# Performance work log

Hardware: AMD Instinct MI355X
Metric: run time of the kernel (lower is better)

## Reference

```python
import jax, jax.numpy as jnp
import numpy as np

B, M, N, R, FIN, D, H = 16, 512, 512, 8, 4, 256, 4
DH = D // H
LGAT = 2
TF_RATE, THRESH = 0.9, 2.0
GAT_W, ORG_W, DET_W = 0.5, 0.5, 0.5


def setup_inputs() -> dict:
    key = jax.random.key(0)
    ks = jax.random.split(key, 16)
    g = lambda k, shp, fan: jax.random.normal(k, shp, jnp.float32) / np.sqrt(fan)
    inp = {
        'tracks': jax.random.normal(ks[0], (B, M, R, FIN), jnp.float32),
        'detections': jax.random.normal(ks[1], (B, N, FIN), jnp.float32),
        'tracklet_marks': jax.random.randint(ks[2], (B,), M // 2, M + 1, jnp.int32),
        'detection_marks': jax.random.randint(ks[3], (B,), N // 2, N + 1, jnp.int32),
        'feat_W1': g(ks[4], (FIN, D), FIN),
        'feat_b1': jnp.zeros((D,), jnp.float32),
        'feat_W2': g(ks[5], (D, D), D),
        'feat_b2': jnp.zeros((D,), jnp.float32),
        'enc_Wqkv': g(ks[6], (D, 3 * D), D),
        'enc_Wo': g(ks[7], (D, D), D),
        'enc_ff1': g(ks[8], (D, 4 * D), D),
        'enc_ff2': g(ks[9], (4 * D, D), 4 * D),
        'gat_W': g(ks[10], (LGAT, D, D), D),
        'gat_a': g(ks[11], (LGAT, 2, H, DH), DH),
        'det_gat_W': g(ks[12], (LGAT, D, D), D),
        'det_gat_a': g(ks[13], (LGAT, 2, H, DH), DH),
        'cls_Wq': g(ks[14], (2, D, D), D),
        'cls_Wk': g(ks[15], (2, D, D), D),
    }
    return inp


def _ln(x):
    m = jnp.mean(x, -1, keepdims=True)
    v = jnp.var(x, -1, keepdims=True)
    return (x - m) * jax.lax.rsqrt(v + 1e-5)


def _feat(x, W1, b1, W2, b2):
    return jax.nn.elu(x @ W1 + b1) @ W2 + b2


def _encoder(x, Wqkv, Wo, ff1, ff2):
    # x: [T, R, D] -> one pre-LN transformer layer over the rewind axis
    T = x.shape[0]
    h = _ln(x)
    qkv = (h @ Wqkv).reshape(T, R, 3, H, DH)
    q, k, v = qkv[:, :, 0], qkv[:, :, 1], qkv[:, :, 2]
    att = jax.nn.softmax(jnp.einsum('trhd,tshd->thrs', q, k) / np.sqrt(DH), axis=-1)
    o = jnp.einsum('thrs,tshd->trhd', att, v).reshape(T, R, D) @ Wo
    x = x + o
    return x + jax.nn.relu(_ln(x) @ ff1) @ ff2


def _gat(x, adj, W, a):
    # x: [B, Nn, D]; adj: [B, Nn, Nn] bool; a: [2, H, DH]
    b, nn_, _ = x.shape
    h = (x @ W).reshape(b, nn_, H, DH)
    src = jnp.einsum('bnhd,hd->bnh', h, a[0])
    dst = jnp.einsum('bnhd,hd->bnh', h, a[1])
    e = jax.nn.leaky_relu(src[:, :, None, :] + dst[:, None, :, :], 0.2)  # [B,Nn,Nn,H]
    e = jnp.where(adj[..., None], e, -1e9)
    alpha = jax.nn.softmax(e, axis=2)
    out = jnp.einsum('bijh,bjhd->bihd', alpha, h).reshape(b, nn_, D)
    return jax.nn.elu(out)


def _scores(x, adj_f, Wq, Wk):
    s = jax.nn.sigmoid(jnp.einsum('bid,bjd->bij', x @ Wq, x @ Wk) / np.sqrt(D))
    return s * adj_f


def _forward(tracks, detections, tracklet_marks, detection_marks,
             feat_W1, feat_b1, feat_W2, feat_b2,
             enc_Wqkv, enc_Wo, enc_ff1, enc_ff2,
             gat_W, gat_a, det_gat_W, det_gat_a, cls_Wq, cls_Wk):
    tr_emb = _feat(tracks, feat_W1, feat_b1, feat_W2, feat_b2)      # [B,M,R,D]
    det_emb = _feat(detections, feat_W1, feat_b1, feat_W2, feat_b2)  # [B,N,D]

    enc = _encoder(tr_emb.reshape(B * M, R, D), enc_Wqkv, enc_Wo, enc_ff1, enc_ff2)
    enc = enc.reshape(B, M, R, D)
    predicted = tr_emb[:, :, 0, :] + TF_RATE * enc[:, :, 0, :]       # [B,M,D]

    tmask = jnp.arange(M)[None, :] < tracklet_marks[:, None]
    dmask = jnp.arange(N)[None, :] < detection_marks[:, None]

    pos = jnp.concatenate([tracks[:, :, 0, :2], detections[:, :, :2]], axis=1)  # [B,M+N,2]
    vmask = jnp.concatenate([tmask, dmask], axis=1)
    dist = jnp.linalg.norm(pos[:, :, None, :] - pos[:, None, :, :], axis=-1)
    adj = (dist < THRESH) & vmask[:, :, None] & vmask[:, None, :]
    adj_f = adj.astype(jnp.float32)

    feat0 = jnp.concatenate([predicted, det_emb], axis=1)  # [B,M+N,D]
    x = feat0
    for l in range(LGAT):
        x = GAT_W * _gat(x, adj, gat_W[l], gat_a[l]) + ORG_W * feat0
    scores = _scores(x, adj_f, cls_Wq[0], cls_Wk[0])       # [B,M+N,M+N]
    asso_results = scores[:, :M, M:]                        # track->det block

    pd = detections[:, :, :2]
    dist_d = jnp.linalg.norm(pd[:, :, None, :] - pd[:, None, :, :], axis=-1)
    adj_d = (dist_d < THRESH) & dmask[:, :, None] & dmask[:, None, :]
    adj_d_f = adj_d.astype(jnp.float32)

    xd = det_emb
    for l in range(LGAT):
        xd = DET_W * _gat(xd, adj_d, det_gat_W[l], det_gat_a[l]) + ORG_W * det_emb
    det_scores = _scores(xd, adj_d_f, cls_Wq[1], cls_Wk[1])
    det_scores = det_scores * (1.0 - jnp.eye(N, dtype=jnp.float32))  # zero_diag

    return scores, det_scores, asso_results


def reference(tracks, detections, tracklet_marks, detection_marks,
              feat_W1, feat_b1, feat_W2, feat_b2,
              enc_Wqkv, enc_Wo, enc_ff1, enc_ff2,
              gat_W, gat_a, det_gat_W, det_gat_a, cls_Wq, cls_Wk):
    return _forward(tracks, detections, tracklet_marks, detection_marks,
                    feat_W1, feat_b1, feat_W2, feat_b2,
                    enc_Wqkv, enc_Wo, enc_ff1, enc_ff2,
                    gat_W, gat_a, det_gat_W, det_gat_a, cls_Wq, cls_Wk)
```

## Files before the change

kernel.cpp:

```cpp
#include <hip/hip_runtime.h>
#include <math.h>


typedef __bf16 bf16;
typedef __bf16 bf16x8 __attribute__((ext_vector_type(8)));
typedef __bf16 bf16x4 __attribute__((ext_vector_type(4)));
typedef float f32x4 __attribute__((ext_vector_type(4)));

__device__ __forceinline__ float bf2f(bf16 x) { return (float)x; }
__device__ __forceinline__ bf16 f2bf(float x) { return (bf16)x; }

__device__ __forceinline__ unsigned encf(float f) {
    unsigned u = __float_as_uint(f);
    return (u & 0x80000000u) ? ~u : (u | 0x80000000u);
}
__device__ __forceinline__ float decf(unsigned u) {
    return (u & 0x80000000u) ? __uint_as_float(u & 0x7fffffffu)
                             : __uint_as_float(~u);
}

__device__ __forceinline__ bool node_adj(float4 a, float4 c) {
    float dx = a.x - c.x, dy = a.y - c.y;
    return (sqrtf(dx * dx + dy * dy) + a.z + c.z) < 2.0f;
}

struct PrepEnt { const float* src; long dofs; int R; int C; int tstart; };
struct PrepTab { PrepEnt e[13]; };

__global__ __launch_bounds__(256) void k_prep(PrepTab tab, bf16* __restrict__ dst)
{
    __shared__ float tile[32][33];
    const int tid = blockIdx.x;
    int k = 0;
    #pragma unroll
    for (int q = 1; q < 13; ++q) if (tid >= tab.e[q].tstart) k = q;
    PrepEnt E = tab.e[k];
    const int local = tid - E.tstart;
    const int cT = E.C >> 5;
    const int tr = local / cT, tc = local - tr * cT;
    const int r0 = tr << 5, c0 = tc << 5;
    const int t = threadIdx.x;
    {
        int r = t >> 3, cq = (t & 7) * 4;
        *(float4*)&tile[r][cq] = *(const float4*)(E.src + (long)(r0 + r) * E.C + c0 + cq);
    }
    __syncthreads();
    {
        int c = t >> 3, rq = (t & 7) * 4;
        bf16x4 o;
        o[0] = f2bf(tile[rq + 0][c]); o[1] = f2bf(tile[rq + 1][c]);
        o[2] = f2bf(tile[rq + 2][c]); o[3] = f2bf(tile[rq + 3][c]);
        *(bf16x4*)(dst + E.dofs + (long)(c0 + c) * E.R + r0 + rq) = o;
    }
}

__device__ __forceinline__ void gemm_bt_mn(const bf16* __restrict__ A, int lda,
                                           const bf16* __restrict__ BT, int ldb,
                                           int K, int m0, int n0, f32x4 acc[4])
{
    __shared__ bf16 As[64][40];
    __shared__ bf16 Bs[64][40];
    const int t = threadIdx.x;
    const int lane = t & 63, wv = t >> 6, lr = lane & 15, kq = lane >> 4;
    const int arow = t >> 2, acol = (t & 3) * 8;
    for (int k0 = 0; k0 < K; k0 += 32) {
        __syncthreads();
        *(uint4*)&As[arow][acol] = *(const uint4*)(A + (long)(m0 + arow) * lda + k0 + acol);
        *(uint4*)&Bs[arow][acol] = *(const uint4*)(BT + (long)(n0 + arow) * ldb + k0 + acol);
        __syncthreads();
        bf16x8 af = *(const bf16x8*)&As[wv * 16 + lr][kq * 8];
        #pragma unroll
        for (int nt = 0; nt < 4; ++nt) {
            bf16x8 bfr = *(const bf16x8*)&Bs[nt * 16 + lr][kq * 8];
            acc[nt] = __builtin_amdgcn_mfma_f32_16x16x32_bf16(af, bfr, acc[nt], 0, 0, 0);
        }
    }
}

__device__ __forceinline__ void gemm_bt(const bf16* __restrict__ A, int lda,
                                        const bf16* __restrict__ BT, int ldb,
                                        int K, f32x4 acc[4])
{
    gemm_bt_mn(A, lda, BT, ldb, K, blockIdx.y * 64, blockIdx.x * 64, acc);
}

__device__ __forceinline__ void gemm128_core(const bf16* __restrict__ A, int lda,
                                             const bf16* __restrict__ BT, int ldb,
                                             int m0, int n0, int K, f32x4 acc[2][8])
{
    __shared__ bf16 As[128][40];
    __shared__ bf16 Bs[128][40];
    const int t = threadIdx.x;
    const int lane = t & 63, wv = t >> 6, lr = lane & 15, kq = lane >> 4;
    const int srow = t >> 1, scol = (t & 1) * 16;
    for (int k0 = 0; k0 < K; k0 += 32) {
        __syncthreads();
        {
            const bf16* ap = A + (long)(m0 + srow) * lda + k0 + scol;
            *(uint4*)&As[srow][scol] = *(const uint4*)ap;
            *(uint4*)&As[srow][scol + 8] = *(const uint4*)(ap + 8);
            const bf16* bp = BT + (long)(n0 + srow) * ldb + k0 + scol;
            *(uint4*)&Bs[srow][scol] = *(const uint4*)bp;
            *(uint4*)&Bs[srow][scol + 8] = *(const uint4*)(bp + 8);
        }
        __syncthreads();
        bf16x8 af[2];
        af[0] = *(const bf16x8*)&As[wv * 32 + lr][kq * 8];
        af[1] = *(const bf16x8*)&As[wv * 32 + 16 + lr][kq * 8];
        #pragma unroll
        for (int nt = 0; nt < 8; ++nt) {
            bf16x8 bfr = *(const bf16x8*)&Bs[nt * 16 + lr][kq * 8];
            acc[0][nt] = __builtin_amdgcn_mfma_f32_16x16x32_bf16(af[0], bfr, acc[0][nt], 0, 0, 0);
            acc[1][nt] = __builtin_amdgcn_mfma_f32_16x16x32_bf16(af[1], bfr, acc[1][nt], 0, 0, 0);
        }
    }
}

__global__ __launch_bounds__(256) void k_gemm128_bf16(
    const bf16* __restrict__ A, int lda,
    const bf16* __restrict__ BT, int ldb,
    bf16* __restrict__ out, int ldo, int K, int relu)
{
    f32x4 acc[2][8] = {};
    const int m0 = blockIdx.y * 128, n0 = blockIdx.x * 128;
    gemm128_core(A, lda, BT, ldb, m0, n0, K, acc);
    const int lane = threadIdx.x & 63, wv = threadIdx.x >> 6;
    const int lr = lane & 15, kq = lane >> 4;
    #pragma unroll
    for (int mt = 0; mt < 2; ++mt) {
        #pragma unroll
        for (int nt = 0; nt < 8; ++nt) {
            int col = n0 + nt * 16 + lr;
            #pragma unroll
            for (int i = 0; i < 4; ++i) {
                int row = m0 + wv * 32 + mt * 16 + kq * 4 + i;
                float v = acc[mt][nt][i];
                if (relu) v = fmaxf(v, 0.f);
                out[(long)row * ldo + col] = f2bf(v);
            }
        }
    }
}

__global__ __launch_bounds__(256) void k_kvq(
    const bf16* __restrict__ hln, const bf16* __restrict__ WqkvT,
    bf16* __restrict__ kv, bf16* __restrict__ q)
{
    const int bid = blockIdx.x;
    const bf16* A; const bf16* BT; bf16* out;
    int lda, ldo, m0, n0;
    if (bid < 2048) {
        A = hln; lda = 256; BT = WqkvT + 65536;
        m0 = (bid >> 2) * 128; n0 = (bid & 3) * 128;
        out = kv; ldo = 512;
    } else {
        int t2 = bid - 2048;
        A = hln; lda = 2048; BT = WqkvT;
        m0 = (t2 >> 1) * 128; n0 = (t2 & 1) * 128;
        out = q; ldo = 256;
    }
    f32x4 acc[2][8] = {};
    gemm128_core(A, lda, BT, 256, m0, n0, 256, acc);
    const int lane = threadIdx.x & 63, wv = threadIdx.x >> 6;
    const int lr = lane & 15, kq = lane >> 4;
    #pragma unroll
    for (int mt = 0; mt < 2; ++mt) {
        #pragma unroll
        for (int nt = 0; nt < 8; ++nt) {
            int col = n0 + nt * 16 + lr;
            #pragma unroll
            for (int i = 0; i < 4; ++i) {
                int row = m0 + wv * 32 + mt * 16 + kq * 4 + i;
                out[(long)row * ldo + col] = f2bf(acc[mt][nt][i]);
            }
        }
    }
}

__global__ __launch_bounds__(256) void k_logits(
    const bf16* __restrict__ xqkm, const bf16* __restrict__ xqkd,
    const unsigned long long* __restrict__ adjmM,
    const unsigned long long* __restrict__ adjmD,
    float* __restrict__ out, float* __restrict__ asso)
{
    const int bid = blockIdx.x;
    const bf16* xqk; float* ob; const unsigned long long* adjm;
    int ldo, nN, nC, flags, m0, n0, z;
    long sAz, sOz;
    if (bid < 1024) {
        z = bid >> 6; int r = bid & 63;
        m0 = (r >> 3) * 128; n0 = (r & 7) * 128;
        xqk = xqkm; sAz = 524288; ob = out; ldo = 1024; sOz = 1048576;
        adjm = adjmM; nN = 1024; nC = 16; flags = 1;
    } else {
        int b2 = bid - 1024;
        z = b2 >> 4; int r = b2 & 15;
        m0 = (r >> 2) * 128; n0 = (r & 3) * 128;
        xqk = xqkd; sAz = 262144; ob = out + 16777216; ldo = 512; sOz = 262144;
        adjm = adjmD; nN = 512; nC = 8; flags = 2;
    }
    f32x4 acc[2][8] = {};
    gemm128_core(xqk + z * sAz, 512, xqk + z * sAz + 256, 512, m0, n0, 256, acc);
    const int lane = threadIdx.x & 63, wv = threadIdx.x >> 6;
    const int lr = lane & 15, kq = lane >> 4;
    float* obz = ob + z * sOz;
    #pragma unroll
    for (int mt = 0; mt < 2; ++mt) {
        #pragma unroll
        for (int i = 0; i < 4; ++i) {
            int row = m0 + wv * 32 + mt * 16 + kq * 4 + i;
            unsigned long long w0 = adjm[((long)z * nN + row) * nC + (n0 >> 6)];
            unsigned long long w1 = adjm[((long)z * nN + row) * nC + (n0 >> 6) + 1];
            #pragma unroll
            for (int nt = 0; nt < 8; ++nt) {
                int col = n0 + nt * 16 + lr;
                int bp = nt * 16 + lr;
                bool adj = (bp < 64) ? ((w0 >> bp) & 1ull) : ((w1 >> (bp - 64)) & 1ull);
                if ((flags & 2) && row == col) adj = false;
                float v = 0.f;
                if (adj) v = 1.f / (1.f + __expf(-acc[mt][nt][i] * 0.0625f));
                obz[(long)row * ldo + col] = v;
                if ((flags & 1) && row < 512 && col >= 512)
                    asso[(long)z * 262144 + (long)row * 512 + (col - 512)] = v;
            }
        }
    }
}

__global__ __launch_bounds__(256) void k_cls(
    const bf16* __restrict__ Am, const bf16* __restrict__ QKm, bf16* __restrict__ outm,
    const bf16* __restrict__ Ad, const bf16* __restrict__ QKd, bf16* __restrict__ outd)
{
    int by = blockIdx.y;
    const bf16 *A, *BT; bf16* out;
    if (by < 256) { A = Am; BT = QKm; out = outm; }
    else          { by -= 256; A = Ad; BT = QKd; out = outd; }
    f32x4 acc[4] = {};
    const int m0 = by * 64, n0 = blockIdx.x * 64;
    gemm_bt_mn(A, 256, BT, 256, 256, m0, n0, acc);
    const int lane = threadIdx.x & 63, wv = threadIdx.x >> 6;
    const int lr = lane & 15, kq = lane >> 4;
    #pragma unroll
    for (int nt = 0; nt < 4; ++nt) {
        int col = n0 + nt * 16 + lr;
        #pragma unroll
        for (int i = 0; i < 4; ++i) {
            int row = m0 + wv * 16 + kq * 4 + i;
            out[(long)row * 512 + col] = f2bf(acc[nt][i]);
        }
    }
}

__global__ __launch_bounds__(256) void k_gemm_pred(
    const bf16* __restrict__ A, int lda,
    const bf16* __restrict__ BT, int ldb,
    const float* __restrict__ res1, const float* __restrict__ res2,
    float* __restrict__ outf, bf16* __restrict__ outb, int K)
{
    f32x4 acc[4] = {};
    gemm_bt(A, lda, BT, ldb, K, acc);
    const int lane = threadIdx.x & 63, wv = threadIdx.x >> 6;
    const int lr = lane & 15, kq = lane >> 4;
    const int m0 = blockIdx.y * 64, n0 = blockIdx.x * 64;
    #pragma unroll
    for (int nt = 0; nt < 4; ++nt) {
        int col = n0 + nt * 16 + lr;
        #pragma unroll
        for (int i = 0; i < 4; ++i) {
            int row = m0 + wv * 16 + kq * 4 + i;
            float v = res1[(long)row * 256 + col]
                    + 0.9f * (res2[(long)row * 256 + col] + acc[nt][i]);
            long drow = (long)row + ((row >> 9) << 9);
            long o = drow * 256 + col;
            outf[o] = v;
            outb[o] = f2bf(v);
        }
    }
}

__global__ __launch_bounds__(256) void k_featgemm(
    const float* __restrict__ tracks, const float* __restrict__ dets,
    const float* __restrict__ W1, const float* __restrict__ b1,
    const bf16* __restrict__ W2T, const float* __restrict__ b2,
    bf16* __restrict__ hln, float* __restrict__ emb_r0_f,
    float* __restrict__ feat0_f, bf16* __restrict__ feat0_b,
    bf16* __restrict__ demb_b)
{
    __shared__ float xr[64][4];
    __shared__ float w1s[4][256];
    __shared__ float b1s[256];
    __shared__ bf16 As[64][40];
    __shared__ bf16 Bs[256][40];
    const int t = threadIdx.x;
    const int m0 = blockIdx.x * 64;
    if (t < 64) {
        int gr = m0 + t;
        const float* sp = (gr < 65536) ? (tracks + (long)gr * 4)
                                       : (dets + (long)(gr - 65536) * 4);
        *(float4*)&xr[t][0] = *(const float4*)sp;
    }
    w1s[0][t] = W1[t];       w1s[1][t] = W1[256 + t];
    w1s[2][t] = W1[512 + t]; w1s[3][t] = W1[768 + t];
    b1s[t] = b1[t];
    const int arow = t >> 2, acol = (t & 3) * 8;
    const int lane = t & 63, wv = t >> 6, lr = lane & 15, kq = lane >> 4;
    f32x4 acc[16] = {};
    __syncthreads();
    for (int k0 = 0; k0 < 256; k0 += 32) {
        __syncthreads();
        #pragma unroll
        for (int j = 0; j < 8; ++j) {
            int c = k0 + acol + j;
            float v = fmaf(xr[arow][0], w1s[0][c],
                      fmaf(xr[arow][1], w1s[1][c],
                      fmaf(xr[arow][2], w1s[2][c],
                      fmaf(xr[arow][3], w1s[3][c], b1s[c]))));
            v = v > 0.f ? v : (__expf(v) - 1.f);
            As[arow][acol + j] = f2bf(v);
        }
        #pragma unroll
        for (int rr = 0; rr < 4; ++rr) {
            int n = rr * 64 + (t >> 2);
            *(uint4*)&Bs[n][acol] = *(const uint4*)(W2T + (long)n * 256 + k0 + acol);
        }
        __syncthreads();
        bf16x8 af = *(const bf16x8*)&As[wv * 16 + lr][kq * 8];
        #pragma unroll
        for (int nt = 0; nt < 16; ++nt) {
            bf16x8 bfr = *(const bf16x8*)&Bs[nt * 16 + lr][kq * 8];
            acc[nt] = __builtin_amdgcn_mfma_f32_16x16x32_bf16(af, bfr, acc[nt], 0, 0, 0);
        }
    }
    if (m0 < 65536) {
        #pragma unroll
        for (int nt = 0; nt < 16; ++nt) {
            int col = nt * 16 + lr;
            float bv = b2[col];
            #pragma unroll
            for (int i = 0; i < 4; ++i) {
                int gr = m0 + wv * 16 + kq * 4 + i;
                float v = acc[nt][i] + bv;
                if ((gr & 7) == 0) emb_r0_f[(long)(gr >> 3) * 256 + col] = v;
                acc[nt][i] = bf2f(f2bf(v));
            }
        }
        float mean[4], rstd[4];
        #pragma unroll
        for (int i = 0; i < 4; ++i) {
            float s1 = 0.f, s2 = 0.f;
            #pragma unroll
            for (int nt = 0; nt < 16; ++nt) {
                float v = acc[nt][i];
                s1 += v; s2 += v * v;
            }
            #pragma unroll
            for (int o = 1; o < 16; o <<= 1) {
                s1 += __shfl_xor(s1, o, 64);
                s2 += __shfl_xor(s2, o, 64);
            }
            float mu = s1 * (1.f / 256.f);
            mean[i] = mu;
            rstd[i] = rsqrtf(fmaxf(s2 * (1.f / 256.f) - mu * mu, 0.f) + 1e-5f);
        }
        #pragma unroll
        for (int nt = 0; nt < 16; ++nt) {
            int col = nt * 16 + lr;
            #pragma unroll
            for (int i = 0; i < 4; ++i) {
                int gr = m0 + wv * 16 + kq * 4 + i;
                hln[(long)gr * 256 + col] = f2bf((acc[nt][i] - mean[i]) * rstd[i]);
            }
        }
    } else {
        #pragma unroll
        for (int nt = 0; nt < 16; ++nt) {
            int col = nt * 16 + lr;
            float bv = b2[col];
            #pragma unroll
            for (int i = 0; i < 4; ++i) {
                int gr = m0 + wv * 16 + kq * 4 + i;
                float v = acc[nt][i] + bv;
                int dr = gr - 65536;
                long drow = ((long)(dr >> 9) << 10) + 512 + (dr & 511);
                feat0_f[drow * 256 + col] = v;
                feat0_b[drow * 256 + col] = f2bf(v);
                demb_b[(long)dr * 256 + col] = f2bf(v);
            }
        }
    }
}

__global__ __launch_bounds__(256) void k_adjmask(
    const float4* __restrict__ nodes,
    unsigned long long* __restrict__ adjm_main,
    unsigned long long* __restrict__ adjm_det)
{
    int bi, nN, nLog, nodeOfs;
    unsigned long long* adjm;
    if (blockIdx.x < 16384) { bi = blockIdx.x; nN = 1024; nLog = 10; nodeOfs = 0; adjm = adjm_main; }
    else { bi = blockIdx.x - 16384; nN = 512; nLog = 9; nodeOfs = 512; adjm = adjm_det; }
    const int b = bi >> nLog;
    const int i = bi & (nN - 1);
    const float4* nb = nodes + b * 1024 + nodeOfs;
    const float4 ni = nb[i];
    const int t = threadIdx.x;
    const int w = t >> 6, lane = t & 63;
    const int nC = nN >> 6;
    for (int it = 0; it * 256 < nN; ++it) {
        int j = it * 256 + t;
        bool adj = node_adj(ni, nb[j]);
        unsigned long long mask = __ballot(adj);
        if (lane == 0) adjm[(long)bi * nC + it * 4 + w] = mask;
    }
}

__global__ __launch_bounds__(256) void k_addres_ln(
    const bf16* __restrict__ A, const bf16* __restrict__ BT,
    const float* __restrict__ res1,
    float* __restrict__ x2out, bf16* __restrict__ h2)
{
    __shared__ bf16 As[64][40];
    __shared__ bf16 Bs[256][40];
    const int t = threadIdx.x;
    const int m0 = blockIdx.x * 64;
    const int arow = t >> 2, acol = (t & 3) * 8;
    const int lane = t & 63, wv = t >> 6, lr = lane & 15, kq = lane >> 4;
    f32x4 acc[16] = {};
    for (int k0 = 0; k0 < 256; k0 += 32) {
        __syncthreads();
        *(uint4*)&As[arow][acol] = *(const uint4*)(A + (long)(m0 + arow) * 256 + k0 + acol);
        #pragma unroll
        for (int rr = 0; rr < 4; ++rr) {
            int n = rr * 64 + (t >> 2);
            *(uint4*)&Bs[n][acol] = *(const uint4*)(BT + (long)n * 256 + k0 + acol);
        }
        __syncthreads();
        bf16x8 af = *(const bf16x8*)&As[wv * 16 + lr][kq * 8];
        #pragma unroll
        for (int nt = 0; nt < 16; ++nt) {
            bf16x8 bfr = *(const bf16x8*)&Bs[nt * 16 + lr][kq * 8];
            acc[nt] = __builtin_amdgcn_mfma_f32_16x16x32_bf16(af, bfr, acc[nt], 0, 0, 0);
        }
    }
    float mean[4], rstd[4];
    #pragma unroll
    for (int i = 0; i < 4; ++i) {
        int row = m0 + wv * 16 + kq * 4 + i;
        float s1 = 0.f, s2 = 0.f;
        #pragma unroll
        for (int nt = 0; nt < 16; ++nt) {
            float v = res1[(long)row * 256 + nt * 16 + lr] + acc[nt][i];
            acc[nt][i] = v;
            s1 += v; s2 += v * v;
        }
        #pragma unroll
        for (int o = 1; o < 16; o <<= 1) {
            s1 += __shfl_xor(s1, o, 64);
            s2 += __shfl_xor(s2, o, 64);
        }
        float mu = s1 * (1.f / 256.f);
        mean[i] = mu;
        rstd[i] = rsqrtf(fmaxf(s2 * (1.f / 256.f) - mu * mu, 0.f) + 1e-5f);
    }
    #pragma unroll
    for (int nt = 0; nt < 16; ++nt) {
        int col = nt * 16 + lr;
        #pragma unroll
        for (int i = 0; i < 4; ++i) {
            int row = m0 + wv * 16 + kq * 4 + i;
            float v = acc[nt][i];
            x2out[(long)row * 256 + col] = v;
            h2[(long)row * 256 + col] = f2bf((v - mean[i]) * rstd[i]);
        }
    }
}

__global__ __launch_bounds__(256) void k_attn(
    const bf16* __restrict__ q, const bf16* __restrict__ kv,
    bf16* __restrict__ o0)
{
    const long t = blockIdx.x;
    const int h = threadIdx.x >> 6;
    const int lane = threadIdx.x & 63;
    const int s = lane >> 3;
    const int dg = lane & 7;
    const bf16* qp = q + t * 256 + h * 64 + dg * 8;
    const bf16* kp = kv + (t * 8 + s) * 512 + h * 64 + dg * 8;
    float p = 0.f;
    #pragma unroll
    for (int e = 0; e < 8; ++e) p += bf2f(qp[e]) * bf2f(kp[e]);
    p += __shfl_xor(p, 1, 64);
    p += __shfl_xor(p, 2, 64);
    p += __shfl_xor(p, 4, 64);
    float sc = p * 0.125f;
    float w[8];
    float mx = -1e30f;
    #pragma unroll
    for (int s2 = 0; s2 < 8; ++s2) { w[s2] = __shfl(sc, s2 * 8, 64); mx = fmaxf(mx, w[s2]); }
    float sum = 0.f;
    #pragma unroll
    for (int s2 = 0; s2 < 8; ++s2) { w[s2] = __expf(w[s2] - mx); sum += w[s2]; }
    float rs = 1.f / sum;
    float acc = 0.f;
    const bf16* vp = kv + (t * 8) * 512 + 256 + h * 64 + lane;
    #pragma unroll
    for (int s2 = 0; s2 < 8; ++s2) acc += w[s2] * bf2f(vp[(long)s2 * 512]);
    o0[t * 256 + h * 64 + lane] = f2bf(acc * rs);
}

__global__ __launch_bounds__(256) void k_nodes(
    const float* __restrict__ tracks, const float* __restrict__ dets,
    const int* __restrict__ tm, const int* __restrict__ dm,
    float4* __restrict__ nodes, unsigned* __restrict__ maxd_all)
{
    int idx = blockIdx.x * 256 + threadIdx.x;
    if (blockIdx.x == 0) maxd_all[threadIdx.x] = 0x007fffffu;
    int b = idx >> 10;
    int i = idx & 1023;
    float x, y;
    int valid;
    if (i < 512) {
        long o = (long)(b * 512 + i) * 32;
        x = tracks[o]; y = tracks[o + 1];
        valid = (i < tm[b]) ? 1 : 0;
    } else {
        int n = i - 512;
        long o = (long)(b * 512 + n) * 4;
        x = dets[o]; y = dets[o + 1];
        valid = (n < dm[b]) ? 1 : 0;
    }
    nodes[idx] = make_float4(x, y, valid ? 0.f : 1e9f, 0.f);
}

__global__ __launch_bounds__(256) void k_gemmT_src(
    const bf16* __restrict__ WTm, const bf16* __restrict__ Xm, bf16* __restrict__ hgTm,
    const float* __restrict__ avm, float* __restrict__ srcm, float* __restrict__ dstm,
    unsigned* __restrict__ mxm,
    const bf16* __restrict__ WTd, const bf16* __restrict__ Xd, bf16* __restrict__ hgTd,
    const float* __restrict__ avd, float* __restrict__ srcd, float* __restrict__ dstd,
    unsigned* __restrict__ mxd)
{
    __shared__ float sred[4][2][64];
    int bx = blockIdx.x;
    const bf16 *WT, *X; bf16* hgT; const float* av;
    float *src, *dst; unsigned* mx; int nN, nLog;
    if (bx < 256) { WT = WTm; X = Xm; hgT = hgTm; av = avm; src = srcm; dst = dstm; mx = mxm; nN = 1024; nLog = 10; }
    else { bx -= 256; WT = WTd; X = Xd; hgT = hgTd; av = avd; src = srcd; dst = dstd; mx = mxd; nN = 512; nLog = 9; }
    const int h = blockIdx.y;
    const int d0 = h * 64, n0 = bx * 64;
    f32x4 acc[4] = {};
    gemm_bt_mn(WT, 256, X, 256, 256, d0, n0, acc);
    const int t = threadIdx.x, lane = t & 63, wv = t >> 6, lr = lane & 15, kq = lane >> 4;
    float a0c[4], a1c[4];
    *(float4*)a0c = *(const float4*)(av + h * 64 + wv * 16 + kq * 4);
    *(float4*)a1c = *(const float4*)(av + 256 + h * 64 + wv * 16 + kq * 4);
    #pragma unroll
    for (int nt = 0; nt < 4; ++nt) {
        int node = n0 + nt * 16 + lr;
        int b = node >> nLog;
        int j = node & (nN - 1);
        float p0 = 0.f, p1 = 0.f;
        #pragma unroll
        for (int i = 0; i < 4; ++i) {
            int d = d0 + wv * 16 + kq * 4 + i;
            bf16 vb = f2bf(acc[nt][i]);
            hgT[((long)(b * 256 + d) << nLog) + j] = vb;
            float vr = bf2f(vb);
            p0 += vr * a0c[i];
            p1 += vr * a1c[i];
        }
        p0 += __shfl_xor(p0, 16, 64); p0 += __shfl_xor(p0, 32, 64);
        p1 += __shfl_xor(p1, 16, 64); p1 += __shfl_xor(p1, 32, 64);
        if (kq == 0) { sred[wv][0][nt * 16 + lr] = p0; sred[wv][1][nt * 16 + lr] = p1; }
    }
    __syncthreads();
    if (t < 64) {
        float s0 = sred[0][0][t] + sred[1][0][t] + sred[2][0][t] + sred[3][0][t];
        float s1 = sred[0][1][t] + sred[1][1][t] + sred[2][1][t] + sred[3][1][t];
        int node = n0 + t;
        src[(long)node * 4 + h] = s0;
        dst[(long)node * 4 + h] = s1;
        float m = s1;
        #pragma unroll
        for (int o = 32; o; o >>= 1) m = fmaxf(m, __shfl_xor(m, o, 64));
        if (t == 0) atomicMax(&mx[(n0 >> nLog) * 4 + h], encf(m));
    }
}

__global__ __launch_bounds__(256) void k_gatagg2(
    const bf16* __restrict__ hgTm, const unsigned long long* __restrict__ adjmM,
    const float4* __restrict__ srcM, const unsigned* __restrict__ mxM,
    const float4* __restrict__ dstM, const float* __restrict__ resM, bf16* __restrict__ outM,
    const bf16* __restrict__ hgTd, const unsigned long long* __restrict__ adjmD,
    const float4* __restrict__ srcD, const unsigned* __restrict__ mxD,
    const float4* __restrict__ dstD, const float* __restrict__ resD, bf16* __restrict__ outD)
{
    __shared__ float dstT[4][1024];
    __shared__ unsigned int adjW[32][33];
    int bid = blockIdx.x;
    const bf16* hgT; const unsigned long long* adjm; const float4* srcv;
    const unsigned* mxp; const float4* dstv; const float* res; bf16* outb; int nN;
    if (bid < 512) { hgT = hgTm; adjm = adjmM; srcv = srcM; mxp = mxM; dstv = dstM; res = resM; outb = outM; nN = 1024; }
    else { bid -= 512; hgT = hgTd; adjm = adjmD; srcv = srcD; mxp = mxD; dstv = dstD; res = resD; outb = outD; nN = 512; }
    const int t = threadIdx.x;
    const int nblk = nN >> 5;
    const int b = bid / nblk;
    const int i0 = (bid - b * nblk) << 5;
    const int nC = nN >> 6;
    for (int j = t; j < nN; j += 256) {
        float4 dj = dstv[(long)b * nN + j];
        dstT[0][j] = dj.x; dstT[1][j] = dj.y; dstT[2][j] = dj.z; dstT[3][j] = dj.w;
    }
    for (int idx = t; idx < 32 * nC; idx += 256) {
        int r = idx / nC, c = idx - r * nC;
        unsigned long long v = adjm[((long)b * nN + i0 + r) * nC + c];
        adjW[r][c * 2] = (unsigned)v;
        adjW[r][c * 2 + 1] = (unsigned)(v >> 32);
    }
    __syncthreads();
    const int h = t >> 6, lane = t & 63, lr = lane & 15, kq = lane >> 4;
    const float mdh = decf(mxp[b * 4 + h]);
    float s_r[2], m_r[2], psum[2] = {0.f, 0.f};
    #pragma unroll
    for (int mt = 0; mt < 2; ++mt) {
        long idx = (long)b * nN + i0 + mt * 16 + lr;
        s_r[mt] = ((const float*)(srcv + idx))[h];
        float tmp = s_r[mt] + mdh;
        m_r[mt] = fmaxf(tmp, 0.2f * tmp);
    }
    f32x4 acc[2][4] = {};
    const bf16* hb = hgT + ((long)b * 256 + h * 64) * nN;
    for (int j0 = 0; j0 < nN; j0 += 32) {
        bf16x8 bfr[4];
        #pragma unroll
        for (int nt = 0; nt < 4; ++nt)
            bfr[nt] = *(const bf16x8*)(hb + (long)(nt * 16 + lr) * nN + j0 + kq * 8);
        #pragma unroll
        for (int mt = 0; mt < 2; ++mt) {
            unsigned byte = (adjW[mt * 16 + lr][j0 >> 5] >> (kq * 8)) & 0xffu;
            bf16x8 af;
            float ps = 0.f;
            #pragma unroll
            for (int jj = 0; jj < 8; ++jj) {
                float e = s_r[mt] + dstT[h][j0 + kq * 8 + jj];
                e = fmaxf(e, 0.2f * e);
                e = (byte & (1u << jj)) ? e : -1e9f;
                float p = __expf(e - m_r[mt]);
                af[jj] = f2bf(p);
                ps += p;
            }
            psum[mt] += ps;
            #pragma unroll
            for (int nt = 0; nt < 4; ++nt)
                acc[mt][nt] = __builtin_amdgcn_mfma_f32_16x16x32_bf16(af, bfr[nt], acc[mt][nt], 0, 0, 0);
        }
    }
    float stot[2];
    #pragma unroll
    for (int mt = 0; mt < 2; ++mt) {
        float v = psum[mt];
        v += __shfl_xor(v, 16, 64);
        v += __shfl_xor(v, 32, 64);
        stot[mt] = v;
    }
    #pragma unroll
    for (int mt = 0; mt < 2; ++mt) {
        #pragma unroll
        for (int ii = 0; ii < 4; ++ii) {
            int i = i0 + mt * 16 + kq * 4 + ii;
            long bi = (long)b * nN + i;
            float sv = __shfl(stot[mt], kq * 4 + ii, 64);
            float rs = 1.f / fmaxf(sv, 1e-30f);
            #pragma unroll
            for (int nt = 0; nt < 4; ++nt) {
                int col = h * 64 + nt * 16 + lr;
                float a = acc[mt][nt][ii] * rs;
                float e = a > 0.f ? a : expm1f(a);
                float v = 0.5f * e + 0.5f * res[(long)b * 262144 + (long)i * 256 + col];
                outb[bi * 256 + col] = f2bf(v);
            }
        }
    }
}

extern "C" void kernel_launch(void* const* d_in, const int* in_sizes, int n_in,
                              void* d_out, int out_size, void* d_ws, size_t ws_size,
                              hipStream_t stream)
{
    (void)in_sizes; (void)n_in; (void)out_size; (void)ws_size;
    const float* tracks = (const float*)d_in[0];
    const float* dets   = (const float*)d_in[1];
    const int*  tmarks = (const int*)d_in[2];
    const int*  dmarks = (const int*)d_in[3];
    const float* W1   = (const float*)d_in[4];
    const float* b1   = (const float*)d_in[5];
    const float* W2   = (const float*)d_in[6];
    const float* b2   = (const float*)d_in[7];
    const float* Wqkv = (const float*)d_in[8];
    const float* Wo   = (const float*)d_in[9];
    const float* eff1 = (const float*)d_in[10];
    const float* eff2 = (const float*)d_in[11];
    const float* gatW = (const float*)d_in[12];
    const float* gatA = (const float*)d_in[13];
    const float* dgatW = (const float*)d_in[14];
    const float* dgatA = (const float*)d_in[15];
    const float* clsWq = (const float*)d_in[16];
    const float* clsWk = (const float*)d_in[17];
    float* out = (float*)d_out;

    char* wsb = (char*)d_ws;
    size_t off = 0;
    auto take = [&](size_t bytes) -> char* {
        char* p = wsb + off;
        off += (bytes + 255) & ~(size_t)255;
        return p;
    };
    char* R_emb  = take(37748736);
    char* R_r0   = take(8388608);
    char* R_hln  = take(33554432);
    char* R_v    = take(33554432);
    char* R_gat  = take(25165824);
    char* R_q    = take(4194304);
    char* R_o0   = take(4194304);
    char* R_f0f  = take(16777216);
    char* R_f0b  = take(8388608);
    char* R_demb = take(4194304);
    float4* nodes = (float4*)take(262144);
    float4* src4  = (float4*)take(262144);
    float4* dst4  = (float4*)take(262144);
    unsigned* maxd_all = (unsigned*)take(1024);
    unsigned long long* adjm_main = (unsigned long long*)take(2097152);
    unsigned long long* adjm_det  = (unsigned long long*)take(524288);
    bf16* wbuf = (bf16*)take(2752512);
    float4* srcd4 = (float4*)take(131072);
    float4* dstd4 = (float4*)take(131072);

    float* emb_r0_f = (float*)R_r0;
    bf16*  hln      = (bf16*)R_hln;
    bf16*  kv_b     = (bf16*)d_out;
    bf16*  q_b      = (bf16*)R_q;
    bf16*  o0_b     = (bf16*)R_o0;
    float* x20      = (float*)R_emb;
    bf16*  h2_b     = (bf16*)(R_emb + 8388608);
    bf16*  f1_b     = (bf16*)R_hln;
    float* feat0_f  = (float*)R_f0f;
    bf16*  feat0_b  = (bf16*)R_f0b;
    bf16*  demb_b   = (bf16*)R_demb;
    bf16*  hgT_m    = (bf16*)R_gat;
    bf16*  xga_m    = (bf16*)(R_gat + 8388608);
    bf16*  xgb_m    = (bf16*)(R_gat + 16777216);
    bf16*  hgT_d    = (bf16*)(R_emb + 16777216);
    bf16*  xga_d    = (bf16*)(R_emb + 20971520);
    bf16*  xgb_d    = (bf16*)(R_emb + 25165824);
    bf16*  xqk_m    = (bf16*)R_v;
    bf16*  xqk_d    = (bf16*)(R_v + 16777216);

    bf16* W2T    = wbuf + 0;
    bf16* WqkvT  = wbuf + 65536;
    bf16* WoT    = wbuf + 262144;
    bf16* eff1T  = wbuf + 327680;
    bf16* eff2T  = wbuf + 589824;
    bf16* gatW0T = wbuf + 851968;
    bf16* gatW1T = wbuf + 917504;
    bf16* dgatW0T= wbuf + 983040;
    bf16* dgatW1T= wbuf + 1048576;
    bf16* clsQK0T= wbuf + 1114112;
    bf16* clsQK1T= wbuf + 1245184;
    PrepTab tab;
    tab.e[0]  = { W2,             0,       256,  256,  0    };
    tab.e[1]  = { Wqkv,           65536,   256,  768,  64   };
    tab.e[2]  = { Wo,             262144,  256,  256,  256  };
    tab.e[3]  = { eff1,           327680,  256,  1024, 320  };
    tab.e[4]  = { eff2,           589824,  1024, 256,  576  };
    tab.e[5]  = { gatW,           851968,  256,  256,  832  };
    tab.e[6]  = { gatW + 65536,   917504,  256,  256,  896  };
    tab.e[7]  = { dgatW,          983040,  256,  256,  960  };
    tab.e[8]  = { dgatW + 65536,  1048576, 256,  256,  1024 };
    tab.e[9]  = { clsWq,          1114112, 256,  256,  1088 };
    tab.e[10] = { clsWk,          1179648, 256,  256,  1152 };
    tab.e[11] = { clsWq + 65536,  1245184, 256,  256,  1216 };
    tab.e[12] = { clsWk + 65536,  1310720, 256,  256,  1280 };

    k_prep<<<1344, 256, 0, stream>>>(tab, wbuf);
    k_nodes<<<64, 256, 0, stream>>>(tracks, dets, tmarks, dmarks, nodes, maxd_all);
    k_adjmask<<<24576, 256, 0, stream>>>(nodes, adjm_main, adjm_det);
    k_featgemm<<<1152, 256, 0, stream>>>(tracks, dets, W1, b1, W2T, b2,
        hln, emb_r0_f, feat0_f, feat0_b, demb_b);

    k_kvq<<<2176, 256, 0, stream>>>(hln, WqkvT, kv_b, q_b);
    k_attn<<<8192, 256, 0, stream>>>(q_b, kv_b, o0_b);
    k_addres_ln<<<128, 256, 0, stream>>>(o0_b, WoT, emb_r0_f, x20, h2_b);
    k_gemm128_bf16<<<dim3(8, 64, 1), 256, 0, stream>>>(h2_b, 256, eff1T, 256, f1_b, 1024, 256, 1);
    k_gemm_pred<<<dim3(4, 128, 1), 256, 0, stream>>>(f1_b, 1024, eff2T, 1024, emb_r0_f, x20, feat0_f, feat0_b, 1024);

    k_gemmT_src<<<dim3(384, 4, 1), 256, 0, stream>>>(
        gatW0T, feat0_b, hgT_m, gatA, (float*)src4, (float*)dst4, maxd_all,
        dgatW0T, demb_b, hgT_d, dgatA, (float*)srcd4, (float*)dstd4, maxd_all + 128);
    k_gatagg2<<<768, 256, 0, stream>>>(
        hgT_m, adjm_main, src4, maxd_all, dst4, feat0_f, xga_m,
        hgT_d, adjm_det, srcd4, maxd_all + 128, dstd4, feat0_f + 131072, xga_d);
    k_gemmT_src<<<dim3(384, 4, 1), 256, 0, stream>>>(
        gatW1T, xga_m, hgT_m, gatA + 512, (float*)src4, (float*)dst4, maxd_all + 64,
        dgatW1T, xga_d, hgT_d, dgatA + 512, (float*)srcd4, (float*)dstd4, maxd_all + 192);
    k_gatagg2<<<768, 256, 0, stream>>>(
        hgT_m, adjm_main, src4, maxd_all + 64, dst4, feat0_f, xgb_m,
        hgT_d, adjm_det, srcd4, maxd_all + 192, dstd4, feat0_f + 131072, xgb_d);

    k_cls<<<dim3(8, 384, 1), 256, 0, stream>>>(xgb_m, clsQK0T, xqk_m, xgb_d, clsQK1T, xqk_d);
    k_logits<<<1280, 256, 0, stream>>>(xqk_m, xqk_d, adjm_main, adjm_det,
        out, out + 20971520L);
}
```

Baseline: 498.8 us.

## Fold classifier Wq·Wk^T into one weight, tile adjacency mask, swizzle block order

Precomputes Wq·Wk^T as a single combined weight in a small kernel. The classifier stage now computes only y = x·Wc (N=256 instead of 512) and takes logits as y·x^T, so the Q/K projection GEMM is halved. The adjacency-mask kernel now stages node coordinates in shared memory and builds 32 rows per block instead of one row per block, and it tests squared distance against a precomputed threshold to avoid the sqrt. Several kernels also remap block IDs in an XCD-style interleave for cache locality. Risks are bf16 rounding of the combined weight and an adjacency test that may differ from the old sqrt form at the boundary.

```diff
diff --git a/kernel.cpp b/kernel.cpp
--- a/kernel.cpp
+++ b/kernel.cpp
@@ -19,12 +19,7 @@
                              : __uint_as_float(~u);
 }
 
-__device__ __forceinline__ bool node_adj(float4 a, float4 c) {
-    float dx = a.x - c.x, dy = a.y - c.y;
-    return (sqrtf(dx * dx + dy * dy) + a.z + c.z) < 2.0f;
-}
-
-struct PrepEnt { const float* src; long dofs; int R; int C; int tstart; };
+struct PrepEnt { const float* src; long dofs; int R; int C; int tstart; int trans; };
 struct PrepTab { PrepEnt e[13]; };
 
 __global__ __launch_bounds__(256) void k_prep(PrepTab tab, bf16* __restrict__ dst)
@@ -45,12 +40,18 @@
         *(float4*)&tile[r][cq] = *(const float4*)(E.src + (long)(r0 + r) * E.C + c0 + cq);
     }
     __syncthreads();
-    {
+    if (E.trans) {
         int c = t >> 3, rq = (t & 7) * 4;
         bf16x4 o;
         o[0] = f2bf(tile[rq + 0][c]); o[1] = f2bf(tile[rq + 1][c]);
         o[2] = f2bf(tile[rq + 2][c]); o[3] = f2bf(tile[rq + 3][c]);
         *(bf16x4*)(dst + E.dofs + (long)(c0 + c) * E.R + r0 + rq) = o;
+    } else {
+        int r = t >> 3, cq = (t & 7) * 4;
+        bf16x4 o;
+        o[0] = f2bf(tile[r][cq + 0]); o[1] = f2bf(tile[r][cq + 1]);
+        o[2] = f2bf(tile[r][cq + 2]); o[3] = f2bf(tile[r][cq + 3]);
+        *(bf16x4*)(dst + E.dofs + (long)(r0 + r) * E.C + c0 + cq) = o;
     }
 }
 
@@ -146,15 +147,15 @@
     const bf16* __restrict__ hln, const bf16* __restrict__ WqkvT,
     bf16* __restrict__ kv, bf16* __restrict__ q)
 {
-    const int bid = blockIdx.x;
+    const int wg = (blockIdx.x & 7) * 272 + (blockIdx.x >> 3);
     const bf16* A; const bf16* BT; bf16* out;
     int lda, ldo, m0, n0;
-    if (bid < 2048) {
+    if (wg < 2048) {
         A = hln; lda = 256; BT = WqkvT + 65536;
-        m0 = (bid >> 2) * 128; n0 = (bid & 3) * 128;
+        m0 = (wg >> 2) * 128; n0 = (wg & 3) * 128;
         out = kv; ldo = 512;
     } else {
-        int t2 = bid - 2048;
+        int t2 = wg - 2048;
         A = hln; lda = 2048; BT = WqkvT;
         m0 = (t2 >> 1) * 128; n0 = (t2 & 1) * 128;
         out = q; ldo = 256;
@@ -177,33 +178,109 @@
     }
 }
 
+__global__ __launch_bounds__(256) void k_wcomb(bf16* __restrict__ wb)
+{
+    const int bid = blockIdx.x;
+    const int head = bid >> 4, r = bid & 15;
+    const bf16* A  = wb + 1179648 + head * 131072;
+    const bf16* BT = wb + 1114112 + head * 131072;
+    bf16* out = wb + 1376256 + head * 65536;
+    const int m0 = (r >> 2) * 64, n0 = (r & 3) * 64;
+    f32x4 acc[4] = {};
+    gemm_bt_mn(A, 256, BT, 256, 256, m0, n0, acc);
+    const int lane = threadIdx.x & 63, wv = threadIdx.x >> 6;
+    const int lr = lane & 15, kq = lane >> 4;
+    #pragma unroll
+    for (int nt = 0; nt < 4; ++nt) {
+        int col = n0 + nt * 16 + lr;
+        #pragma unroll
+        for (int i = 0; i < 4; ++i) {
+            int row = m0 + wv * 16 + kq * 4 + i;
+            out[(long)row * 256 + col] = f2bf(acc[nt][i]);
+        }
+    }
+}
+
+__global__ __launch_bounds__(256) void k_y(
+    const bf16* __restrict__ xm, const bf16* __restrict__ WcT0, bf16* __restrict__ ym,
+    const bf16* __restrict__ xd, const bf16* __restrict__ WcT1, bf16* __restrict__ yd)
+{
+    const int wg = (blockIdx.x & 7) * 192 + (blockIdx.x >> 3);
+    int by = wg >> 2;
+    const int bx = wg & 3;
+    const bf16 *A, *BT; bf16* out;
+    if (by < 256) { A = xm; BT = WcT0; out = ym; }
+    else          { by -= 256; A = xd; BT = WcT1; out = yd; }
+    f32x4 acc[4] = {};
+    const int m0 = by * 64, n0 = bx * 64;
+    gemm_bt_mn(A, 256, BT, 256, 256, m0, n0, acc);
+    const int lane = threadIdx.x & 63, wv = threadIdx.x >> 6;
+    const int lr = lane & 15, kq = lane >> 4;
+    #pragma unroll
+    for (int nt = 0; nt < 4; ++nt) {
+        int col = n0 + nt * 16 + lr;
+        #pragma unroll
+        for (int i = 0; i < 4; ++i) {
+            int row = m0 + wv * 16 + kq * 4 + i;
+            out[(long)row * 256 + col] = f2bf(acc[nt][i]);
+        }
+    }
+}
+
 __global__ __launch_bounds__(256) void k_logits(
-    const bf16* __restrict__ xqkm, const bf16* __restrict__ xqkd,
+    const bf16* __restrict__ ym, const bf16* __restrict__ xm,
+    const bf16* __restrict__ yd, const bf16* __restrict__ xd,
     const unsigned long long* __restrict__ adjmM,
     const unsigned long long* __restrict__ adjmD,
     float* __restrict__ out, float* __restrict__ asso)
 {
-    const int bid = blockIdx.x;
-    const bf16* xqk; float* ob; const unsigned long long* adjm;
+    const int wg = (blockIdx.x & 7) * 160 + (blockIdx.x >> 3);
+    const bf16 *A, *BT; float* ob; const unsigned long long* adjm;
     int ldo, nN, nC, flags, m0, n0, z;
-    long sAz, sOz;
-    if (bid < 1024) {
-        z = bid >> 6; int r = bid & 63;
+    if (wg < 1024) {
+        z = wg >> 6; int r = wg & 63;
         m0 = (r >> 3) * 128; n0 = (r & 7) * 128;
-        xqk = xqkm; sAz = 524288; ob = out; ldo = 1024; sOz = 1048576;
+        A = ym + (long)z * 262144; BT = xm + (long)z * 262144;
+        ob = out + (long)z * 1048576; ldo = 1024;
         adjm = adjmM; nN = 1024; nC = 16; flags = 1;
     } else {
-        int b2 = bid - 1024;
-        z = b2 >> 4; int r = b2 & 15;
+        int t2 = wg - 1024;
+        z = t2 >> 4; int r = t2 & 15;
         m0 = (r >> 2) * 128; n0 = (r & 3) * 128;
-        xqk = xqkd; sAz = 262144; ob = out + 16777216; ldo = 512; sOz = 262144;
+        A = yd + (long)z * 131072; BT = xd + (long)z * 131072;
+        ob = out + 16777216 + (long)z * 262144; ldo = 512;
         adjm = adjmD; nN = 512; nC = 8; flags = 2;
     }
+    const int t = threadIdx.x;
+    const int lane = t & 63, wv = t >> 6, lr = lane & 15, kq = lane >> 4;
     f32x4 acc[2][8] = {};
-    gemm128_core(xqk + z * sAz, 512, xqk + z * sAz + 256, 512, m0, n0, 256, acc);
-    const int lane = threadIdx.x & 63, wv = threadIdx.x >> 6;
-    const int lr = lane & 15, kq = lane >> 4;
-    float* obz = ob + z * sOz;
+    {
+        __shared__ bf16 As[128][72];
+        __shared__ bf16 Bs[128][72];
+        const int srow4 = t >> 3, scol8 = (t & 7) * 8;
+        for (int k0 = 0; k0 < 256; k0 += 64) {
+            __syncthreads();
+            #pragma unroll
+            for (int p = 0; p < 4; ++p) {
+                int row = p * 32 + srow4;
+                *(uint4*)&As[row][scol8] = *(const uint4*)(A + (long)(m0 + row) * 256 + k0 + scol8);
+                *(uint4*)&Bs[row][scol8] = *(const uint4*)(BT + (long)(n0 + row) * 256 + k0 + scol8);
+            }
+            __syncthreads();
+            #pragma unroll
+            for (int ks = 0; ks < 64; ks += 32) {
+                bf16x8 af[2];
+                af[0] = *(const bf16x8*)&As[wv * 32 + lr][kq * 8 + ks];
+                af[1] = *(const bf16x8*)&As[wv * 32 + 16 + lr][kq * 8 + ks];
+                #pragma unroll
+                for (int nt = 0; nt < 8; ++nt) {
+                    bf16x8 bfr = *(const bf16x8*)&Bs[nt * 16 + lr][kq * 8 + ks];
+                    acc[0][nt] = __builtin_amdgcn_mfma_f32_16x16x32_bf16(af[0], bfr, acc[0][nt], 0, 0, 0);
+                    acc[1][nt] = __builtin_amdgcn_mfma_f32_16x16x32_bf16(af[1], bfr, acc[1][nt], 0, 0, 0);
+                }
+            }
+        }
+    }
     #pragma unroll
     for (int mt = 0; mt < 2; ++mt) {
         #pragma unroll
@@ -219,34 +296,10 @@
                 if ((flags & 2) && row == col) adj = false;
                 float v = 0.f;
                 if (adj) v = 1.f / (1.f + __expf(-acc[mt][nt][i] * 0.0625f));
-                obz[(long)row * ldo + col] = v;
+                ob[(long)row * ldo + col] = v;
                 if ((flags & 1) && row < 512 && col >= 512)
                     asso[(long)z * 262144 + (long)row * 512 + (col - 512)] = v;
             }
-        }
-    }
-}
-
-__global__ __launch_bounds__(256) void k_cls(
-    const bf16* __restrict__ Am, const bf16* __restrict__ QKm, bf16* __restrict__ outm,
-    const bf16* __restrict__ Ad, const bf16* __restrict__ QKd, bf16* __restrict__ outd)
-{
-    int by = blockIdx.y;
-    const bf16 *A, *BT; bf16* out;
-    if (by < 256) { A = Am; BT = QKm; out = outm; }
-    else          { by -= 256; A = Ad; BT = QKd; out = outd; }
-    f32x4 acc[4] = {};
-    const int m0 = by * 64, n0 = blockIdx.x * 64;
-    gemm_bt_mn(A, 256, BT, 256, 256, m0, n0, acc);
-    const int lane = threadIdx.x & 63, wv = threadIdx.x >> 6;
-    const int lr = lane & 15, kq = lane >> 4;
-    #pragma unroll
-    for (int nt = 0; nt < 4; ++nt) {
-        int col = n0 + nt * 16 + lr;
-        #pragma unroll
-        for (int i = 0; i < 4; ++i) {
-            int row = m0 + wv * 16 + kq * 4 + i;
-            out[(long)row * 512 + col] = f2bf(acc[nt][i]);
         }
     }
 }
@@ -395,22 +448,28 @@
     unsigned long long* __restrict__ adjm_main,
     unsigned long long* __restrict__ adjm_det)
 {
-    int bi, nN, nLog, nodeOfs;
+    __shared__ float4 nds[1024];
+    int bid = blockIdx.x;
+    int nN, b, i0, nodeOfs;
     unsigned long long* adjm;
-    if (blockIdx.x < 16384) { bi = blockIdx.x; nN = 1024; nLog = 10; nodeOfs = 0; adjm = adjm_main; }
-    else { bi = blockIdx.x - 16384; nN = 512; nLog = 9; nodeOfs = 512; adjm = adjm_det; }
-    const int b = bi >> nLog;
-    const int i = bi & (nN - 1);
+    if (bid < 512) { nN = 1024; b = bid >> 5; i0 = (bid & 31) << 5; nodeOfs = 0; adjm = adjm_main; }
+    else { int b2 = bid - 512; nN = 512; b = b2 >> 4; i0 = (b2 & 15) << 5; nodeOfs = 512; adjm = adjm_det; }
     const float4* nb = nodes + b * 1024 + nodeOfs;
-    const float4 ni = nb[i];
     const int t = threadIdx.x;
-    const int w = t >> 6, lane = t & 63;
+    for (int j = t; j < nN; j += 256) nds[j] = nb[j];
+    __syncthreads();
+    const int w = t >> 6, l = t & 63;
     const int nC = nN >> 6;
-    for (int it = 0; it * 256 < nN; ++it) {
-        int j = it * 256 + t;
-        bool adj = node_adj(ni, nb[j]);
-        unsigned long long mask = __ballot(adj);
-        if (lane == 0) adjm[(long)bi * nC + it * 4 + w] = mask;
+    for (int ii = 0; ii < 8; ++ii) {
+        int i = i0 + w * 8 + ii;
+        float4 ni = nds[i];
+        for (int c = 0; c < nC; ++c) {
+            float4 nj = nds[c * 64 + l];
+            float dx = ni.x - nj.x, dy = ni.y - nj.y;
+            bool adj = (dx * dx + dy * dy < 4.f) && (ni.z + nj.z < 1.f);
+            unsigned long long mask = __ballot(adj);
+            if (l == 0) adjm[(long)(b * nN + i) * nC + c] = mask;
+        }
     }
 }
 
@@ -541,12 +600,13 @@
     unsigned* __restrict__ mxd)
 {
     __shared__ float sred[4][2][64];
-    int bx = blockIdx.x;
+    const int wg = (blockIdx.x & 7) * 192 + (blockIdx.x >> 3);
+    const int h = wg & 3;
+    int bx = wg >> 2;
     const bf16 *WT, *X; bf16* hgT; const float* av;
     float *src, *dst; unsigned* mx; int nN, nLog;
     if (bx < 256) { WT = WTm; X = Xm; hgT = hgTm; av = avm; src = srcm; dst = dstm; mx = mxm; nN = 1024; nLog = 10; }
     else { bx -= 256; WT = WTd; X = Xd; hgT = hgTd; av = avd; src = srcd; dst = dstd; mx = mxd; nN = 512; nLog = 9; }
-    const int h = blockIdx.y;
     const int d0 = h * 64, n0 = bx * 64;
     f32x4 acc[4] = {};
     gemm_bt_mn(WT, 256, X, 256, 256, d0, n0, acc);
@@ -597,7 +657,7 @@
 {
     __shared__ float dstT[4][1024];
     __shared__ unsigned int adjW[32][33];
-    int bid = blockIdx.x;
+    int bid = (blockIdx.x & 7) * 96 + (blockIdx.x >> 3);
     const bf16* hgT; const unsigned long long* adjm; const float4* srcv;
     const unsigned* mxp; const float4* dstv; const float* res; bf16* outb; int nN;
     if (bid < 512) { hgT = hgTm; adjm = adjmM; srcv = srcM; mxp = mxM; dstv = dstM; res = resM; outb = outM; nN = 1024; }
@@ -731,7 +791,7 @@
     unsigned* maxd_all = (unsigned*)take(1024);
     unsigned long long* adjm_main = (unsigned long long*)take(2097152);
     unsigned long long* adjm_det  = (unsigned long long*)take(524288);
-    bf16* wbuf = (bf16*)take(2752512);
+    bf16* wbuf = (bf16*)take(3014656);
     float4* srcd4 = (float4*)take(131072);
     float4* dstd4 = (float4*)take(131072);
 
@@ -752,8 +812,8 @@
     bf16*  hgT_d    = (bf16*)(R_emb + 16777216);
     bf16*  xga_d    = (bf16*)(R_emb + 20971520);
     bf16*  xgb_d    = (bf16*)(R_emb + 25165824);
-    bf16*  xqk_m    = (bf16*)R_v;
-    bf16*  xqk_d    = (bf16*)(R_v + 16777216);
+    bf16*  y_m      = (bf16*)R_v;
+    bf16*  y_d      = (bf16*)(R_v + 8388608);
 
     bf16* W2T    = wbuf + 0;
     bf16* WqkvT  = wbuf + 65536;
@@ -764,26 +824,27 @@
     bf16* gatW1T = wbuf + 917504;
     bf16* dgatW0T= wbuf + 983040;
     bf16* dgatW1T= wbuf + 1048576;
-    bf16* clsQK0T= wbuf + 1114112;
-    bf16* clsQK1T= wbuf + 1245184;
+    bf16* WcT0   = wbuf + 1376256;
+    bf16* WcT1   = wbuf + 1441792;
     PrepTab tab;
-    tab.e[0]  = { W2,             0,       256,  256,  0    };
-    tab.e[1]  = { Wqkv,           65536,   256,  768,  64   };
-    tab.e[2]  = { Wo,             262144,  256,  256,  256  };
-    tab.e[3]  = { eff1,           327680,  256,  1024, 320  };
-    tab.e[4]  = { eff2,           589824,  1024, 256,  576  };
-    tab.e[5]  = { gatW,           851968,  256,  256,  832  };
-    tab.e[6]  = { gatW + 65536,   917504,  256,  256,  896  };
-    tab.e[7]  = { dgatW,          983040,  256,  256,  960  };
-    tab.e[8]  = { dgatW + 65536,  1048576, 256,  256,  1024 };
-    tab.e[9]  = { clsWq,          1114112, 256,  256,  1088 };
-    tab.e[10] = { clsWk,          1179648, 256,  256,  1152 };
-    tab.e[11] = { clsWq + 65536,  1245184, 256,  256,  1216 };
-    tab.e[12] = { clsWk + 65536,  1310720, 256,  256,  1280 };
+    tab.e[0]  = { W2,             0,       256,  256,  0,    1 };
+    tab.e[1]  = { Wqkv,           65536,   256,  768,  64,   1 };
+    tab.e[2]  = { Wo,             262144,  256,  256,  256,  1 };
+    tab.e[3]  = { eff1,           327680,  256,  1024, 320,  1 };
+    tab.e[4]  = { eff2,           589824,  1024, 256,  576,  1 };
+    tab.e[5]  = { gatW,           851968,  256,  256,  832,  1 };
+    tab.e[6]  = { gatW + 65536,   917504,  256,  256,  896,  1 };
+    tab.e[7]  = { dgatW,          983040,  256,  256,  960,  1 };
+    tab.e[8]  = { dgatW + 65536,  1048576, 256,  256,  1024, 1 };
+    tab.e[9]  = { clsWq,          1114112, 256,  256,  1088, 0 };
+    tab.e[10] = { clsWk,          1179648, 256,  256,  1152, 0 };
+    tab.e[11] = { clsWq + 65536,  1245184, 256,  256,  1216, 0 };
+    tab.e[12] = { clsWk + 65536,  1310720, 256,  256,  1280, 0 };
 
     k_prep<<<1344, 256, 0, stream>>>(tab, wbuf);
+    k_wcomb<<<32, 256, 0, stream>>>(wbuf);
     k_nodes<<<64, 256, 0, stream>>>(tracks, dets, tmarks, dmarks, nodes, maxd_all);
-    k_adjmask<<<24576, 256, 0, stream>>>(nodes, adjm_main, adjm_det);
+    k_adjmask<<<768, 256, 0, stream>>>(nodes, adjm_main, adjm_det);
     k_featgemm<<<1152, 256, 0, stream>>>(tracks, dets, W1, b1, W2T, b2,
         hln, emb_r0_f, feat0_f, feat0_b, demb_b);
 
@@ -793,20 +854,20 @@
     k_gemm128_bf16<<<dim3(8, 64, 1), 256, 0, stream>>>(h2_b, 256, eff1T, 256, f1_b, 1024, 256, 1);
     k_gemm_pred<<<dim3(4, 128, 1), 256, 0, stream>>>(f1_b, 1024, eff2T, 1024, emb_r0_f, x20, feat0_f, feat0_b, 1024);
 
-    k_gemmT_src<<<dim3(384, 4, 1), 256, 0, stream>>>(
+    k_gemmT_src<<<1536, 256, 0, stream>>>(
         gatW0T, feat0_b, hgT_m, gatA, (float*)src4, (float*)dst4, maxd_all,
         dgatW0T, demb_b, hgT_d, dgatA, (float*)srcd4, (float*)dstd4, maxd_all + 128);
     k_gatagg2<<<768, 256, 0, stream>>>(
         hgT_m, adjm_main, src4, maxd_all, dst4, feat0_f, xga_m,
         hgT_d, adjm_det, srcd4, maxd_all + 128, dstd4, feat0_f + 131072, xga_d);
-    k_gemmT_src<<<dim3(384, 4, 1), 256, 0, stream>>>(
+    k_gemmT_src<<<1536, 256, 0, stream>>>(
         gatW1T, xga_m, hgT_m, gatA + 512, (float*)src4, (float*)dst4, maxd_all + 64,
         dgatW1T, xga_d, hgT_d, dgatA + 512, (float*)srcd4, (float*)dstd4, maxd_all + 192);
     k_gatagg2<<<768, 256, 0, stream>>>(
         hgT_m, adjm_main, src4, maxd_all + 64, dst4, feat0_f, xgb_m,
         hgT_d, adjm_det, srcd4, maxd_all + 192, dstd4, feat0_f + 131072, xgb_d);
 
-    k_cls<<<dim3(8, 384, 1), 256, 0, stream>>>(xgb_m, clsQK0T, xqk_m, xgb_d, clsQK1T, xqk_d);
-    k_logits<<<1280, 256, 0, stream>>>(xqk_m, xqk_d, adjm_main, adjm_det,
+    k_y<<<1536, 256, 0, stream>>>(xgb_m, WcT0, y_m, xgb_d, WcT1, y_d);
+    k_logits<<<1280, 256, 0, stream>>>(y_m, xgb_m, y_d, xgb_d, adjm_main, adjm_det,
         out, out + 20971520L);
 }
```

Measured after the change: 497.2 us. About the same (-0.3%).
